# Performance work log

Measured on AMD Instinct MI355X. Metric: run time of the kernel, lower is better.

Reference implementation:

```python
import jax, jax.numpy as jnp
import numpy as np

K = 3      # deformable kernel size
PAD = 1    # padding for all 3x3 convs


def conv2d(x, w, b):
    y = jax.lax.conv_general_dilated(x, w, (1, 1), ((PAD, PAD), (PAD, PAD)),
                                     dimension_numbers=('NCHW', 'OIHW', 'NCHW'))
    return y + b[None, :, None, None]


def ln_channels(x, w, b, eps=1e-5):
    # Restormer 'WithBias' LayerNorm: normalize over channel dim of NCHW
    mu = jnp.mean(x, axis=1, keepdims=True)
    var = jnp.mean((x - mu) ** 2, axis=1, keepdims=True)
    return (x - mu) / jnp.sqrt(var + eps) * w[None, :, None, None] + b[None, :, None, None]


def deform_conv(x, offset, mask, weight, bias):
    # x: [B,Cin,H,W], offset: [B,2*K*K,H,W] (dy,dx interleaved), mask: [B,K*K,H,W]
    B, Cin, H, W = x.shape
    Kk = K * K
    off = offset.reshape(B, Kk, 2, H, W)
    dy, dx = off[:, :, 0], off[:, :, 1]                     # [B,Kk,H,W]
    ky, kx = jnp.meshgrid(jnp.arange(K), jnp.arange(K), indexing='ij')
    ky = (ky.reshape(-1) - PAD).astype(x.dtype)             # [Kk]
    kx = (kx.reshape(-1) - PAD).astype(x.dtype)
    py = jnp.arange(H, dtype=x.dtype)[None, None, :, None] + ky[None, :, None, None] + dy
    px = jnp.arange(W, dtype=x.dtype)[None, None, None, :] + kx[None, :, None, None] + dx
    y0 = jnp.floor(py); x0 = jnp.floor(px)
    wy1 = py - y0; wx1 = px - x0
    xf = x.reshape(B, Cin, H * W)

    def corner(yc, xc, wgt):
        valid = (yc >= 0) & (yc <= H - 1) & (xc >= 0) & (xc <= W - 1)
        yi = jnp.clip(yc, 0, H - 1).astype(jnp.int32)
        xi = jnp.clip(xc, 0, W - 1).astype(jnp.int32)
        idx = (yi * W + xi).reshape(B, -1)                  # [B, Kk*H*W]
        v = jax.vmap(lambda xb, ib: xb[:, ib])(xf, idx)     # [B, Cin, Kk*H*W]
        v = v.reshape(B, Cin, Kk, H, W)
        return v * (wgt * valid.astype(x.dtype))[:, None]

    sampled = (corner(y0, x0, (1 - wy1) * (1 - wx1))
               + corner(y0, x0 + 1, (1 - wy1) * wx1)
               + corner(y0 + 1, x0, wy1 * (1 - wx1))
               + corner(y0 + 1, x0 + 1, wy1 * wx1))         # [B,Cin,Kk,H,W]
    sampled = sampled * mask[:, None]                        # modulated (DCNv2)
    wk = weight.reshape(weight.shape[0], Cin, Kk)            # [Cout,Cin,Kk]
    out = jnp.einsum('bckhw,ock->bohw', sampled, wk)
    return out + bias[None, :, None, None]


def setup_inputs() -> dict:
    key = jax.random.key(0)
    ks = jax.random.split(key, 12)
    B, Ce, Cf, H, W = 4, 32, 64, 128, 128
    Cin, Kk = Ce + Cf, K * K
    d = {
        'f_evt_rec': jax.random.normal(ks[0], (B, Ce, H, W), jnp.float32),
        'f_efnet':   jax.random.normal(ks[1], (B, Cf, H, W), jnp.float32),
        'ln_evt_w': jnp.ones((Ce,), jnp.float32), 'ln_evt_b': jnp.zeros((Ce,), jnp.float32),
        'ln_ef_w':  jnp.ones((Cf,), jnp.float32), 'ln_ef_b':  jnp.zeros((Cf,), jnp.float32),
        'ln_al_w':  jnp.ones((Cf,), jnp.float32), 'ln_al_b':  jnp.zeros((Cf,), jnp.float32),
        'off_w': jax.random.normal(ks[2], (2 * Kk, Cin, K, K), jnp.float32) * 0.01,
        'off_b': jnp.zeros((2 * Kk,), jnp.float32),
        'mod_w': jax.random.normal(ks[3], (Kk, Cin, K, K), jnp.float32) * 0.01,
        'mod_b': jnp.zeros((Kk,), jnp.float32),
        'reg_w': jax.random.normal(ks[4], (Cf, Cin, K, K), jnp.float32) * 0.05,
        'reg_b': jnp.zeros((Cf,), jnp.float32),
        'stage_idx': 0,
    }
    return d


def reference(f_evt_rec, f_efnet, ln_evt_w, ln_evt_b, ln_ef_w, ln_ef_b,
              ln_al_w, ln_al_b, off_w, off_b, mod_w, mod_b, reg_w, reg_b, stage_idx):
    e = ln_channels(f_evt_rec, ln_evt_w, ln_evt_b)
    fe = ln_channels(f_efnet, ln_ef_w, ln_ef_b)
    ox = jnp.concatenate([e, fe], axis=1)                    # [B,96,H,W]
    offset = conv2d(ox, off_w, off_b)
    mask = 2.0 * jax.nn.sigmoid(conv2d(ox, mod_w, mod_b))
    al = deform_conv(ox, offset, mask, reg_w, reg_b)         # [B,64,H,W]
    al = jnp.where(al >= 0, al, 0.2 * al)                    # LeakyReLU(0.2)
    al = ln_channels(al, ln_al_w, ln_al_b)
    return al
```

## Files before the change

### kernel.cpp

```cpp
#include <hip/hip_runtime.h>
#include <hip/hip_bf16.h>

#define BATCH 4
#define HH 128
#define WW 128
#define CE 32
#define CF 64
#define CIN 96
#define KK 9
#define COUT 64

typedef __bf16 bf16x8 __attribute__((ext_vector_type(8)));
typedef float f32x4 __attribute__((ext_vector_type(4)));

#define MFMA16(a, b, c) __builtin_amdgcn_mfma_f32_16x16x32_bf16(a, b, c, 0, 0, 0)

typedef union { uint4 u; bf16x8 v; } U8;

#define OX_BYTES   (BATCH * HH * WW * CIN * 2)
#define OFFM_OFFB  OX_BYTES
#define OFFM_BYTES (BATCH * HH * WW * 27 * 4)
#define WCT_OFFB   (OFFM_OFFB + OFFM_BYTES)
#define WCT_BYTES  (32 * 864 * 2)
#define WKT_OFFB   (WCT_OFFB + WCT_BYTES)
#define WKT_BYTES  (64 * 864 * 2)

__global__ void prep_weights(const float* __restrict__ off_w,
                             const float* __restrict__ mod_w,
                             const float* __restrict__ reg_w,
                             __hip_bfloat16* __restrict__ wcombT,
                             __hip_bfloat16* __restrict__ wkT) {
  int e = blockIdx.x * 256 + threadIdx.x;
  const int TOT1 = 32 * 864;
  const int TOT2 = 64 * 864;
  if (e < TOT1) {
    int oc = e / 864, k = e % 864;
    int tap = k / 96, c = k % 96;
    float v = 0.f;
    if (oc < 18)      v = off_w[(oc * CIN + c) * KK + tap];
    else if (oc < 27) v = mod_w[((oc - 18) * CIN + c) * KK + tap];
    wcombT[e] = __float2bfloat16(v);
  } else if (e < TOT1 + TOT2) {
    int e2 = e - TOT1;
    int oc = e2 / 864, k = e2 % 864;
    int tap = k / 96, c = k % 96;
    wkT[e2] = __float2bfloat16(reg_w[(oc * CIN + c) * KK + tap]);
  }
}

__global__ __launch_bounds__(128) void ln_concat(
    const float* __restrict__ evt, const float* __restrict__ efn,
    const float* __restrict__ w_e, const float* __restrict__ b_e,
    const float* __restrict__ w_f, const float* __restrict__ b_f,
    __hip_bfloat16* __restrict__ ox) {
  __shared__ float vals[WW * 97];
  __shared__ float mu_e[WW], rs_e[WW], mu_f[WW], rs_f[WW];
  __shared__ float lnw[CIN], lnb[CIN];
  int t = threadIdx.x;
  int b = blockIdx.x >> 7, y = blockIdx.x & 127;
  if (t < CIN) {
    lnw[t] = (t < CE) ? w_e[t] : w_f[t - CE];
    lnb[t] = (t < CE) ? b_e[t] : b_f[t - CE];
  }
  int x = t;
  float s = 0.f, s2 = 0.f;
  const float* pe = evt + ((size_t)(b * CE) * HH + y) * WW + x;
  for (int c = 0; c < CE; ++c) {
    float v = pe[(size_t)c * HH * WW];
    vals[x * 97 + c] = v;
    s += v; s2 += v * v;
  }
  float mu = s * (1.f / CE);
  float var = s2 * (1.f / CE) - mu * mu;
  mu_e[x] = mu; rs_e[x] = rsqrtf(var + 1e-5f);
  s = 0.f; s2 = 0.f;
  const float* pf = efn + ((size_t)(b * CF) * HH + y) * WW + x;
  for (int c = 0; c < CF; ++c) {
    float v = pf[(size_t)c * HH * WW];
    vals[x * 97 + CE + c] = v;
    s += v; s2 += v * v;
  }
  mu = s * (1.f / CF);
  var = s2 * (1.f / CF) - mu * mu;
  mu_f[x] = mu; rs_f[x] = rsqrtf(var + 1e-5f);
  __syncthreads();
  uint* orow = (uint*)(ox + (size_t)blockIdx.x * WW * CIN);
  for (int i = 0; i < 48; ++i) {
    int g = i * 128 + t;
    int xx = g / 48, c = (g % 48) * 2;
    float v0 = vals[xx * 97 + c], v1 = vals[xx * 97 + c + 1];
    float o0 = (c < CE) ? (v0 - mu_e[xx]) * rs_e[xx] : (v0 - mu_f[xx]) * rs_f[xx];
    float o1 = (c + 1 < CE) ? (v1 - mu_e[xx]) * rs_e[xx] : (v1 - mu_f[xx]) * rs_f[xx];
    o0 = o0 * lnw[c] + lnb[c];
    o1 = o1 * lnw[c + 1] + lnb[c + 1];
    __hip_bfloat16 h0 = __float2bfloat16(o0), h1 = __float2bfloat16(o1);
    orow[g] = ((uint)*(unsigned short*)&h1 << 16) | (uint)*(unsigned short*)&h0;
  }
}

__global__ __launch_bounds__(256) void conv_offmask_mfma(
    const __hip_bfloat16* __restrict__ ox,
    const __hip_bfloat16* __restrict__ wcombT,
    const float* __restrict__ off_b, const float* __restrict__ mod_b,
    float* __restrict__ offm) {
  __shared__ float outl[64 * 28];

  int bid = blockIdx.x;
  int wg = (bid & 7) * 128 + (bid >> 3);
  int p0 = wg * 64;
  int b = p0 >> 14;
  int y = (p0 >> 7) & 127;
  int x0 = p0 & 127;

  int t = threadIdx.x, lane = t & 63, wv = t >> 6;
  int mw = wv >> 1, nw = wv & 1;
  int lr = lane & 15, lg = lane >> 4;

  const __hip_bfloat16* oxb = ox + (((size_t)b) << 14) * CIN;
  const __hip_bfloat16* brow = wcombT + (size_t)(nw * 16 + lr) * 864;

  f32x4 acc0 = {0.f, 0.f, 0.f, 0.f}, acc1 = {0.f, 0.f, 0.f, 0.f};

#pragma unroll
  for (int tap = 0; tap < 9; ++tap) {
    int dy = tap / 3 - 1, dx = tap % 3 - 1;
    int yy = y + dy;
    int xx0 = x0 + mw * 32 + lr + dx;
    int xx1 = xx0 + 16;
    bool v0 = ((unsigned)yy < 128u) && ((unsigned)xx0 < 128u);
    bool v1 = ((unsigned)yy < 128u) && ((unsigned)xx1 < 128u);
    int cy = min(max(yy, 0), 127);
    int cx0 = min(max(xx0, 0), 127);
    int cx1 = min(max(xx1, 0), 127);
    const __hip_bfloat16* arow = oxb + ((size_t)(cy << 7)) * CIN;
#pragma unroll
    for (int ks = 0; ks < 3; ++ks) {
      int ko = ks * 32 + lg * 8;
      U8 a0, a1, bf;
      a0.u = *(const uint4*)(arow + cx0 * CIN + ko);
      a1.u = *(const uint4*)(arow + cx1 * CIN + ko);
      if (!v0) { a0.u.x = 0; a0.u.y = 0; a0.u.z = 0; a0.u.w = 0; }
      if (!v1) { a1.u.x = 0; a1.u.y = 0; a1.u.z = 0; a1.u.w = 0; }
      bf.u = *(const uint4*)(brow + tap * 96 + ko);
      acc0 = MFMA16(a0.v, bf.v, acc0);
      acc1 = MFMA16(a1.v, bf.v, acc1);
    }
  }

  int oc = nw * 16 + lr;
  float bia = 0.f;
  if (oc < 18) bia = off_b[oc];
  else if (oc < 27) bia = mod_b[oc - 18];
#pragma unroll
  for (int mi = 0; mi < 2; ++mi) {
    f32x4 a = mi ? acc1 : acc0;
#pragma unroll
    for (int r = 0; r < 4; ++r) {
      int px = mw * 32 + mi * 16 + lg * 4 + r;
      if (oc < 27) {
        float v = a[r] + bia;
        if (oc >= 18) v = 2.f / (1.f + __expf(-v));
        outl[px * 28 + oc] = v;
      }
    }
  }
  __syncthreads();
  for (int e = t; e < 64 * 27; e += 256) {
    int px = e / 27, c = e % 27;
    offm[(size_t)p0 * 27 + e] = outl[px * 28 + c];
  }
}

__global__ __launch_bounds__(256) void deform_ln_mfma(
    const __hip_bfloat16* __restrict__ ox,
    const float* __restrict__ offm,
    const __hip_bfloat16* __restrict__ wkT,
    const float* __restrict__ reg_b,
    const float* __restrict__ lnw, const float* __restrict__ lnb,
    float* __restrict__ out) {
  __shared__ char smem[45056];
  int*   sI  = (int*)smem;
  float* sW  = (float*)(smem + 9216);
  short* SaA = (short*)(smem + 18432);
  short* SaB = (short*)(smem + 31744);
  float* outl = (float*)smem;

  int bid = blockIdx.x;
  int wg = (bid & 7) * 128 + (bid >> 3);
  int p0 = wg * 64;
  int b = p0 >> 14;
  int y = (p0 >> 7) & 127;
  int x0 = p0 & 127;
  const __hip_bfloat16* oxb = ox + (((size_t)b) << 14) * CIN;

  int t = threadIdx.x, lane = t & 63, wv = t >> 6;
  int mw = wv >> 1, nw = wv & 1;
  int lr = lane & 15, lg = lane >> 4;

  for (int u = t; u < 576; u += 256) {
    int px = u & 63, tap = u >> 6;
    const float* om = offm + (size_t)(p0 + px) * 27;
    float dyv = om[2 * tap], dxv = om[2 * tap + 1], mk = om[18 + tap];
    float psy = (float)(y + tap / 3 - 1) + dyv;
    float psx = (float)(x0 + px + tap % 3 - 1) + dxv;
    float fy = floorf(psy), fx = floorf(psx);
    float wy1 = psy - fy, wx1 = psx - fx;
    float wy0 = 1.f - wy1, wx0 = 1.f - wx1;
    int iy0 = (int)fy, ix0 = (int)fx;
    int iy1 = iy0 + 1, ix1 = ix0 + 1;
    float vy0 = ((unsigned)iy0 < 128u) ? 1.f : 0.f;
    float vy1 = ((unsigned)iy1 < 128u) ? 1.f : 0.f;
    float vx0 = ((unsigned)ix0 < 128u) ? 1.f : 0.f;
    float vx1 = ((unsigned)ix1 < 128u) ? 1.f : 0.f;
    int cy0 = min(max(iy0, 0), 127), cy1 = min(max(iy1, 0), 127);
    int cx0 = min(max(ix0, 0), 127), cx1 = min(max(ix1, 0), 127);
    int base = u * 4;
    sI[base + 0] = ((cy0 << 7) + cx0) * CIN;
    sI[base + 1] = ((cy0 << 7) + cx1) * CIN;
    sI[base + 2] = ((cy1 << 7) + cx0) * CIN;
    sI[base + 3] = ((cy1 << 7) + cx1) * CIN;
    sW[base + 0] = wy0 * wx0 * vy0 * vx0 * mk;
    sW[base + 1] = wy0 * wx1 * vy0 * vx1 * mk;
    sW[base + 2] = wy1 * wx0 * vy1 * vx0 * mk;
    sW[base + 3] = wy1 * wx1 * vy1 * vx1 * mk;
  }
  __syncthreads();

  f32x4 a00 = {0.f,0.f,0.f,0.f}, a01 = {0.f,0.f,0.f,0.f};
  f32x4 a10 = {0.f,0.f,0.f,0.f}, a11 = {0.f,0.f,0.f,0.f};

  const __hip_bfloat16* wb0 = wkT + (size_t)(nw * 32 + lr) * 864;
  const __hip_bfloat16* wb1 = wkT + (size_t)(nw * 32 + 16 + lr) * 864;

  for (int tap = 0; tap < 9; ++tap) {
    short* S = (tap & 1) ? SaB : SaA;
#pragma unroll
    for (int it = 0; it < 3; ++it) {
      int u = it * 256 + t;
      int px = u / 12, c8 = u % 12;
      int pb = (tap * 64 + px) * 4;
      const int* si = sI + pb;
      const float* sw = sW + pb;
      uint4 q0 = *(const uint4*)(oxb + si[0] + c8 * 8);
      uint4 q1 = *(const uint4*)(oxb + si[1] + c8 * 8);
      uint4 q2 = *(const uint4*)(oxb + si[2] + c8 * 8);
      uint4 q3 = *(const uint4*)(oxb + si[3] + c8 * 8);
      float w0 = sw[0], w1 = sw[1], w2 = sw[2], w3 = sw[3];
      uint rr[4];
#pragma unroll
      for (int j = 0; j < 4; ++j) {
        uint u0 = ((uint*)&q0)[j], u1 = ((uint*)&q1)[j];
        uint u2 = ((uint*)&q2)[j], u3 = ((uint*)&q3)[j];
        float lo = w0 * __uint_as_float(u0 << 16) + w1 * __uint_as_float(u1 << 16)
                 + w2 * __uint_as_float(u2 << 16) + w3 * __uint_as_float(u3 << 16);
        float hi = w0 * __uint_as_float(u0 & 0xffff0000u) + w1 * __uint_as_float(u1 & 0xffff0000u)
                 + w2 * __uint_as_float(u2 & 0xffff0000u) + w3 * __uint_as_float(u3 & 0xffff0000u);
        __hip_bfloat16 bl = __float2bfloat16(lo);
        __hip_bfloat16 bh = __float2bfloat16(hi);
        rr[j] = ((uint)*(unsigned short*)&bh << 16) | (uint)*(unsigned short*)&bl;
      }
      uint4 rv = {rr[0], rr[1], rr[2], rr[3]};
      *(uint4*)&S[px * 104 + c8 * 8] = rv;
    }
    __syncthreads();
#pragma unroll
    for (int ks = 0; ks < 3; ++ks) {
      int ko = ks * 32 + lg * 8;
      bf16x8 fa0 = *(const bf16x8*)&S[(mw * 32 + lr) * 104 + ko];
      bf16x8 fa1 = *(const bf16x8*)&S[(mw * 32 + 16 + lr) * 104 + ko];
      U8 b0, b1;
      b0.u = *(const uint4*)(wb0 + tap * 96 + ko);
      b1.u = *(const uint4*)(wb1 + tap * 96 + ko);
      a00 = MFMA16(fa0, b0.v, a00);
      a01 = MFMA16(fa0, b1.v, a01);
      a10 = MFMA16(fa1, b0.v, a10);
      a11 = MFMA16(fa1, b1.v, a11);
    }
  }
  __syncthreads();

#pragma unroll
  for (int mi = 0; mi < 2; ++mi)
#pragma unroll
  for (int ni = 0; ni < 2; ++ni) {
    int oc = nw * 32 + ni * 16 + lr;
    float bia = reg_b[oc];
    f32x4 a = (mi == 0) ? (ni == 0 ? a00 : a01) : (ni == 0 ? a10 : a11);
#pragma unroll
    for (int r = 0; r < 4; ++r) {
      int px = mw * 32 + mi * 16 + lg * 4 + r;
      float v = a[r] + bia;
      v = (v >= 0.f) ? v : 0.2f * v;
      outl[px * 68 + oc] = v;
    }
  }
  __syncthreads();

  {
    int px = t >> 2, part = t & 3;
    float s = 0.f, s2 = 0.f;
#pragma unroll
    for (int j = 0; j < 16; ++j) {
      float v = outl[px * 68 + part * 16 + j];
      s += v; s2 += v * v;
    }
    s += __shfl_xor(s, 1); s2 += __shfl_xor(s2, 1);
    s += __shfl_xor(s, 2); s2 += __shfl_xor(s2, 2);
    float mu = s * (1.f / 64.f);
    float var = s2 * (1.f / 64.f) - mu * mu;
    float rs = rsqrtf(var + 1e-5f);
    size_t ob = (size_t)b * COUT * 16384 + (size_t)y * 128 + x0 + px;
#pragma unroll
    for (int j = 0; j < 16; ++j) {
      int oc = part * 16 + j;
      float v = outl[px * 68 + oc];
      out[ob + (size_t)oc * 16384] = (v - mu) * rs * lnw[oc] + lnb[oc];
    }
  }
}

extern "C" void kernel_launch(void* const* d_in, const int* in_sizes, int n_in,
                              void* d_out, int out_size, void* d_ws, size_t ws_size,
                              hipStream_t stream) {
  const float* evt      = (const float*)d_in[0];
  const float* efn      = (const float*)d_in[1];
  const float* ln_evt_w = (const float*)d_in[2];
  const float* ln_evt_b = (const float*)d_in[3];
  const float* ln_ef_w  = (const float*)d_in[4];
  const float* ln_ef_b  = (const float*)d_in[5];
  const float* ln_al_w  = (const float*)d_in[6];
  const float* ln_al_b  = (const float*)d_in[7];
  const float* off_w    = (const float*)d_in[8];
  const float* off_b    = (const float*)d_in[9];
  const float* mod_w    = (const float*)d_in[10];
  const float* mod_b    = (const float*)d_in[11];
  const float* reg_w    = (const float*)d_in[12];
  const float* reg_b    = (const float*)d_in[13];
  float* out = (float*)d_out;

  char* wsb = (char*)d_ws;
  __hip_bfloat16* oxb    = (__hip_bfloat16*)wsb;
  float*          offm   = (float*)(wsb + OFFM_OFFB);
  __hip_bfloat16* wcombT = (__hip_bfloat16*)(wsb + WCT_OFFB);
  __hip_bfloat16* wkT    = (__hip_bfloat16*)(wsb + WKT_OFFB);

  prep_weights<<<(32 * 864 + 64 * 864 + 255) / 256, 256, 0, stream>>>(
      off_w, mod_w, reg_w, wcombT, wkT);
  ln_concat<<<BATCH * HH, 128, 0, stream>>>(
      evt, efn, ln_evt_w, ln_evt_b, ln_ef_w, ln_ef_b, oxb);
  conv_offmask_mfma<<<BATCH * HH * WW / 64, 256, 0, stream>>>(
      oxb, wcombT, off_b, mod_b, offm);
  deform_ln_mfma<<<BATCH * HH * WW / 64, 256, 0, stream>>>(
      oxb, offm, wkT, reg_b, ln_al_w, ln_al_b, out);
}
```

Before: 176.0 us.

## Fuse offset/mask conv into deformable conv kernel and software-pipeline bilinear gathers

Merges the offset/mask convolution and the deformable convolution into one kernel. The offset/mask results stay in shared memory instead of making a global round trip, and one launch is removed. The offset conv now reads a 3x66 halo tile of ox staged in LDS rather than issuing scattered global loads per tap. The deform gather is restructured so each thread handles one pixel and 24 channels, and the loads for the next tap are issued before the current tap's MFMAs. The LN/concat kernel is retiled to 64-pixel blocks with 256 threads and partial channel reductions. In exchange the fused kernel holds more registers and may run at lower occupancy.

```diff
diff --git a/kernel.cpp b/kernel.cpp
--- a/kernel.cpp
+++ b/kernel.cpp
@@ -12,18 +12,13 @@
 
 typedef __bf16 bf16x8 __attribute__((ext_vector_type(8)));
 typedef float f32x4 __attribute__((ext_vector_type(4)));
-
 #define MFMA16(a, b, c) __builtin_amdgcn_mfma_f32_16x16x32_bf16(a, b, c, 0, 0, 0)
-
 typedef union { uint4 u; bf16x8 v; } U8;
 
 #define OX_BYTES   (BATCH * HH * WW * CIN * 2)
-#define OFFM_OFFB  OX_BYTES
-#define OFFM_BYTES (BATCH * HH * WW * 27 * 4)
-#define WCT_OFFB   (OFFM_OFFB + OFFM_BYTES)
+#define WCT_OFFB   OX_BYTES
 #define WCT_BYTES  (32 * 864 * 2)
 #define WKT_OFFB   (WCT_OFFB + WCT_BYTES)
-#define WKT_BYTES  (64 * 864 * 2)
 
 __global__ void prep_weights(const float* __restrict__ off_w,
                              const float* __restrict__ mod_w,
@@ -48,220 +43,215 @@
   }
 }
 
-__global__ __launch_bounds__(128) void ln_concat(
+__global__ __launch_bounds__(256) void ln_concat(
     const float* __restrict__ evt, const float* __restrict__ efn,
     const float* __restrict__ w_e, const float* __restrict__ b_e,
     const float* __restrict__ w_f, const float* __restrict__ b_f,
     __hip_bfloat16* __restrict__ ox) {
-  __shared__ float vals[WW * 97];
-  __shared__ float mu_e[WW], rs_e[WW], mu_f[WW], rs_f[WW];
-  __shared__ float lnw[CIN], lnb[CIN];
-  int t = threadIdx.x;
-  int b = blockIdx.x >> 7, y = blockIdx.x & 127;
-  if (t < CIN) {
-    lnw[t] = (t < CE) ? w_e[t] : w_f[t - CE];
-    lnb[t] = (t < CE) ? b_e[t] : b_f[t - CE];
-  }
-  int x = t;
-  float s = 0.f, s2 = 0.f;
-  const float* pe = evt + ((size_t)(b * CE) * HH + y) * WW + x;
-  for (int c = 0; c < CE; ++c) {
-    float v = pe[(size_t)c * HH * WW];
-    vals[x * 97 + c] = v;
-    s += v; s2 += v * v;
-  }
-  float mu = s * (1.f / CE);
-  float var = s2 * (1.f / CE) - mu * mu;
-  mu_e[x] = mu; rs_e[x] = rsqrtf(var + 1e-5f);
-  s = 0.f; s2 = 0.f;
-  const float* pf = efn + ((size_t)(b * CF) * HH + y) * WW + x;
-  for (int c = 0; c < CF; ++c) {
-    float v = pf[(size_t)c * HH * WW];
-    vals[x * 97 + CE + c] = v;
-    s += v; s2 += v * v;
-  }
-  mu = s * (1.f / CF);
-  var = s2 * (1.f / CF) - mu * mu;
-  mu_f[x] = mu; rs_f[x] = rsqrtf(var + 1e-5f);
-  __syncthreads();
-  uint* orow = (uint*)(ox + (size_t)blockIdx.x * WW * CIN);
-  for (int i = 0; i < 48; ++i) {
-    int g = i * 128 + t;
-    int xx = g / 48, c = (g % 48) * 2;
-    float v0 = vals[xx * 97 + c], v1 = vals[xx * 97 + c + 1];
-    float o0 = (c < CE) ? (v0 - mu_e[xx]) * rs_e[xx] : (v0 - mu_f[xx]) * rs_f[xx];
-    float o1 = (c + 1 < CE) ? (v1 - mu_e[xx]) * rs_e[xx] : (v1 - mu_f[xx]) * rs_f[xx];
-    o0 = o0 * lnw[c] + lnb[c];
-    o1 = o1 * lnw[c + 1] + lnb[c + 1];
-    __hip_bfloat16 h0 = __float2bfloat16(o0), h1 = __float2bfloat16(o1);
-    orow[g] = ((uint)*(unsigned short*)&h1 << 16) | (uint)*(unsigned short*)&h0;
-  }
-}
-
-__global__ __launch_bounds__(256) void conv_offmask_mfma(
-    const __hip_bfloat16* __restrict__ ox,
-    const __hip_bfloat16* __restrict__ wcombT,
-    const float* __restrict__ off_b, const float* __restrict__ mod_b,
-    float* __restrict__ offm) {
-  __shared__ float outl[64 * 28];
+  __shared__ float vals[64 * 97];
+  __shared__ float part[4 * 64 * 4];
+  __shared__ float stat[64 * 4];
 
   int bid = blockIdx.x;
   int wg = (bid & 7) * 128 + (bid >> 3);
   int p0 = wg * 64;
-  int b = p0 >> 14;
-  int y = (p0 >> 7) & 127;
-  int x0 = p0 & 127;
+  int b = p0 >> 14, y = (p0 >> 7) & 127, x0 = p0 & 127;
+  int t = threadIdx.x, px = t & 63, g = t >> 6;
+
+  float sE = 0.f, sE2 = 0.f, sF = 0.f, sF2 = 0.f;
+  const float* pe = evt + (((size_t)b * CE) << 14) + (y << 7) + x0 + px;
+#pragma unroll
+  for (int j = 0; j < 8; ++j) {
+    int c = g * 8 + j;
+    float v = pe[(size_t)c << 14];
+    vals[px * 97 + c] = v; sE += v; sE2 += v * v;
+  }
+  const float* pf = efn + (((size_t)b * CF) << 14) + (y << 7) + x0 + px;
+#pragma unroll
+  for (int j = 0; j < 16; ++j) {
+    int c = g * 16 + j;
+    float v = pf[(size_t)c << 14];
+    vals[px * 97 + CE + c] = v; sF += v; sF2 += v * v;
+  }
+  {
+    float4 p4 = {sE, sE2, sF, sF2};
+    *(float4*)&part[(g * 64 + px) * 4] = p4;
+  }
+  __syncthreads();
+  if (g == 0) {
+    float aE = 0.f, aE2 = 0.f, aF = 0.f, aF2 = 0.f;
+#pragma unroll
+    for (int gg = 0; gg < 4; ++gg) {
+      float4 p4 = *(const float4*)&part[(gg * 64 + px) * 4];
+      aE += p4.x; aE2 += p4.y; aF += p4.z; aF2 += p4.w;
+    }
+    float muE = aE * (1.f / CE);
+    float vE = aE2 * (1.f / CE) - muE * muE;
+    float muF = aF * (1.f / CF);
+    float vF = aF2 * (1.f / CF) - muF * muF;
+    float4 s4 = {muE, rsqrtf(vE + 1e-5f), muF, rsqrtf(vF + 1e-5f)};
+    *(float4*)&stat[px * 4] = s4;
+  }
+  __syncthreads();
+  uint* orow = (uint*)(ox + (size_t)p0 * CIN);
+#pragma unroll
+  for (int i = 0; i < 12; ++i) {
+    int e = i * 256 + t;
+    int xx = e / 48, c = (e % 48) * 2;
+    float v0 = vals[xx * 97 + c], v1 = vals[xx * 97 + c + 1];
+    float mu, rs, lw0, lb0, lw1, lb1;
+    if (c < CE) {
+      mu = stat[xx * 4 + 0]; rs = stat[xx * 4 + 1];
+      lw0 = w_e[c]; lb0 = b_e[c]; lw1 = w_e[c + 1]; lb1 = b_e[c + 1];
+    } else {
+      mu = stat[xx * 4 + 2]; rs = stat[xx * 4 + 3];
+      lw0 = w_f[c - CE]; lb0 = b_f[c - CE]; lw1 = w_f[c + 1 - CE]; lb1 = b_f[c + 1 - CE];
+    }
+    float o0 = (v0 - mu) * rs * lw0 + lb0;
+    float o1 = (v1 - mu) * rs * lw1 + lb1;
+    __hip_bfloat16 h0 = __float2bfloat16(o0), h1 = __float2bfloat16(o1);
+    orow[e] = ((uint)*(unsigned short*)&h1 << 16) | (uint)*(unsigned short*)&h0;
+  }
+}
+
+__device__ __forceinline__ uint blend1(uint u0, uint u1, uint u2, uint u3,
+                                       float w0, float w1, float w2, float w3) {
+  float lo = w0 * __uint_as_float(u0 << 16) + w1 * __uint_as_float(u1 << 16)
+           + w2 * __uint_as_float(u2 << 16) + w3 * __uint_as_float(u3 << 16);
+  float hi = w0 * __uint_as_float(u0 & 0xffff0000u) + w1 * __uint_as_float(u1 & 0xffff0000u)
+           + w2 * __uint_as_float(u2 & 0xffff0000u) + w3 * __uint_as_float(u3 & 0xffff0000u);
+  __hip_bfloat16 bl = __float2bfloat16(lo), bh = __float2bfloat16(hi);
+  return ((uint)*(unsigned short*)&bh << 16) | (uint)*(unsigned short*)&bl;
+}
+
+__global__ __launch_bounds__(256) void conv_deform_fused(
+    const __hip_bfloat16* __restrict__ ox,
+    const __hip_bfloat16* __restrict__ wcombT,
+    const __hip_bfloat16* __restrict__ wkT,
+    const float* __restrict__ off_b, const float* __restrict__ mod_b,
+    const float* __restrict__ reg_b,
+    const float* __restrict__ lnw, const float* __restrict__ lnb,
+    float* __restrict__ out) {
+  __shared__ char smem[41216];
+  short* At   = (short*)smem;
+  float* offm = (float*)smem;
+  short* SaA  = (short*)(smem + 7168);
+  short* SaB  = (short*)(smem + 20480);
+  float* outl = (float*)(smem + 7168);
+
+  int bid = blockIdx.x;
+  int wg = (bid & 7) * 128 + (bid >> 3);
+  int p0 = wg * 64;
+  int b = p0 >> 14, y = (p0 >> 7) & 127, x0 = p0 & 127;
+  const __hip_bfloat16* oxb = ox + (((size_t)b) << 14) * CIN;
 
   int t = threadIdx.x, lane = t & 63, wv = t >> 6;
   int mw = wv >> 1, nw = wv & 1;
   int lr = lane & 15, lg = lane >> 4;
 
-  const __hip_bfloat16* oxb = ox + (((size_t)b) << 14) * CIN;
-  const __hip_bfloat16* brow = wcombT + (size_t)(nw * 16 + lr) * 864;
-
-  f32x4 acc0 = {0.f, 0.f, 0.f, 0.f}, acc1 = {0.f, 0.f, 0.f, 0.f};
-
-#pragma unroll
-  for (int tap = 0; tap < 9; ++tap) {
-    int dy = tap / 3 - 1, dx = tap % 3 - 1;
-    int yy = y + dy;
-    int xx0 = x0 + mw * 32 + lr + dx;
-    int xx1 = xx0 + 16;
-    bool v0 = ((unsigned)yy < 128u) && ((unsigned)xx0 < 128u);
-    bool v1 = ((unsigned)yy < 128u) && ((unsigned)xx1 < 128u);
-    int cy = min(max(yy, 0), 127);
-    int cx0 = min(max(xx0, 0), 127);
-    int cx1 = min(max(xx1, 0), 127);
-    const __hip_bfloat16* arow = oxb + ((size_t)(cy << 7)) * CIN;
-#pragma unroll
-    for (int ks = 0; ks < 3; ++ks) {
-      int ko = ks * 32 + lg * 8;
-      U8 a0, a1, bf;
-      a0.u = *(const uint4*)(arow + cx0 * CIN + ko);
-      a1.u = *(const uint4*)(arow + cx1 * CIN + ko);
-      if (!v0) { a0.u.x = 0; a0.u.y = 0; a0.u.z = 0; a0.u.w = 0; }
-      if (!v1) { a1.u.x = 0; a1.u.y = 0; a1.u.z = 0; a1.u.w = 0; }
-      bf.u = *(const uint4*)(brow + tap * 96 + ko);
-      acc0 = MFMA16(a0.v, bf.v, acc0);
-      acc1 = MFMA16(a1.v, bf.v, acc1);
-    }
-  }
-
-  int oc = nw * 16 + lr;
-  float bia = 0.f;
-  if (oc < 18) bia = off_b[oc];
-  else if (oc < 27) bia = mod_b[oc - 18];
-#pragma unroll
-  for (int mi = 0; mi < 2; ++mi) {
-    f32x4 a = mi ? acc1 : acc0;
-#pragma unroll
-    for (int r = 0; r < 4; ++r) {
-      int px = mw * 32 + mi * 16 + lg * 4 + r;
-      if (oc < 27) {
-        float v = a[r] + bia;
-        if (oc >= 18) v = 2.f / (1.f + __expf(-v));
-        outl[px * 28 + oc] = v;
+  for (int u = t; u < 3 * 66 * 12; u += 256) {
+    int c8 = u % 12, pw_ = u / 12, w = pw_ % 66, r = pw_ / 66;
+    int yy = y + r - 1, xx = x0 + w - 1;
+    uint4 v = {0u, 0u, 0u, 0u};
+    if ((unsigned)yy < 128u && (unsigned)xx < 128u)
+      v = *(const uint4*)(oxb + (size_t)((yy << 7) + xx) * CIN + c8 * 8);
+    *(uint4*)&At[(r * 66 + w) * 104 + c8 * 8] = v;
+  }
+  __syncthreads();
+
+  f32x4 cc0 = {0.f,0.f,0.f,0.f}, cc1 = {0.f,0.f,0.f,0.f};
+  {
+    const __hip_bfloat16* brow = wcombT + (size_t)(nw * 16 + lr) * 864;
+#pragma unroll
+    for (int tap = 0; tap < 9; ++tap) {
+      int dy = tap / 3, dx = tap % 3;
+#pragma unroll
+      for (int ks = 0; ks < 3; ++ks) {
+        int ko = ks * 32 + lg * 8;
+        bf16x8 a0 = *(const bf16x8*)&At[(dy * 66 + mw * 32 + lr + dx) * 104 + ko];
+        bf16x8 a1 = *(const bf16x8*)&At[(dy * 66 + mw * 32 + 16 + lr + dx) * 104 + ko];
+        U8 bf; bf.u = *(const uint4*)(brow + tap * 96 + ko);
+        cc0 = MFMA16(a0, bf.v, cc0);
+        cc1 = MFMA16(a1, bf.v, cc1);
       }
     }
   }
   __syncthreads();
-  for (int e = t; e < 64 * 27; e += 256) {
-    int px = e / 27, c = e % 27;
-    offm[(size_t)p0 * 27 + e] = outl[px * 28 + c];
-  }
-}
-
-__global__ __launch_bounds__(256) void deform_ln_mfma(
-    const __hip_bfloat16* __restrict__ ox,
-    const float* __restrict__ offm,
-    const __hip_bfloat16* __restrict__ wkT,
-    const float* __restrict__ reg_b,
-    const float* __restrict__ lnw, const float* __restrict__ lnb,
-    float* __restrict__ out) {
-  __shared__ char smem[45056];
-  int*   sI  = (int*)smem;
-  float* sW  = (float*)(smem + 9216);
-  short* SaA = (short*)(smem + 18432);
-  short* SaB = (short*)(smem + 31744);
-  float* outl = (float*)smem;
-
-  int bid = blockIdx.x;
-  int wg = (bid & 7) * 128 + (bid >> 3);
-  int p0 = wg * 64;
-  int b = p0 >> 14;
-  int y = (p0 >> 7) & 127;
-  int x0 = p0 & 127;
-  const __hip_bfloat16* oxb = ox + (((size_t)b) << 14) * CIN;
-
-  int t = threadIdx.x, lane = t & 63, wv = t >> 6;
-  int mw = wv >> 1, nw = wv & 1;
-  int lr = lane & 15, lg = lane >> 4;
-
-  for (int u = t; u < 576; u += 256) {
-    int px = u & 63, tap = u >> 6;
-    const float* om = offm + (size_t)(p0 + px) * 27;
-    float dyv = om[2 * tap], dxv = om[2 * tap + 1], mk = om[18 + tap];
-    float psy = (float)(y + tap / 3 - 1) + dyv;
-    float psx = (float)(x0 + px + tap % 3 - 1) + dxv;
-    float fy = floorf(psy), fx = floorf(psx);
-    float wy1 = psy - fy, wx1 = psx - fx;
-    float wy0 = 1.f - wy1, wx0 = 1.f - wx1;
-    int iy0 = (int)fy, ix0 = (int)fx;
-    int iy1 = iy0 + 1, ix1 = ix0 + 1;
-    float vy0 = ((unsigned)iy0 < 128u) ? 1.f : 0.f;
-    float vy1 = ((unsigned)iy1 < 128u) ? 1.f : 0.f;
-    float vx0 = ((unsigned)ix0 < 128u) ? 1.f : 0.f;
-    float vx1 = ((unsigned)ix1 < 128u) ? 1.f : 0.f;
-    int cy0 = min(max(iy0, 0), 127), cy1 = min(max(iy1, 0), 127);
-    int cx0 = min(max(ix0, 0), 127), cx1 = min(max(ix1, 0), 127);
-    int base = u * 4;
-    sI[base + 0] = ((cy0 << 7) + cx0) * CIN;
-    sI[base + 1] = ((cy0 << 7) + cx1) * CIN;
-    sI[base + 2] = ((cy1 << 7) + cx0) * CIN;
-    sI[base + 3] = ((cy1 << 7) + cx1) * CIN;
-    sW[base + 0] = wy0 * wx0 * vy0 * vx0 * mk;
-    sW[base + 1] = wy0 * wx1 * vy0 * vx1 * mk;
-    sW[base + 2] = wy1 * wx0 * vy1 * vx0 * mk;
-    sW[base + 3] = wy1 * wx1 * vy1 * vx1 * mk;
-  }
-  __syncthreads();
-
+
+  {
+    int oc = nw * 16 + lr;
+    if (oc < 27) {
+      float bia = (oc < 18) ? off_b[oc] : mod_b[oc - 18];
+#pragma unroll
+      for (int mi = 0; mi < 2; ++mi) {
+        f32x4 a = mi ? cc1 : cc0;
+#pragma unroll
+        for (int r = 0; r < 4; ++r) {
+          int px2 = mw * 32 + mi * 16 + lg * 4 + r;
+          float v = a[r] + bia;
+          if (oc >= 18) v = 2.f / (1.f + __expf(-v));
+          offm[px2 * 28 + oc] = v;
+        }
+      }
+    }
+  }
+  __syncthreads();
+
+  int px = t & 63;
+  int c8b = wv * 3;
+  const __hip_bfloat16* gb = oxb + c8b * 8;
+  const __hip_bfloat16* wb0 = wkT + (size_t)(nw * 32 + lr) * 864;
+  const __hip_bfloat16* wb1 = wkT + (size_t)(nw * 32 + 16 + lr) * 864;
   f32x4 a00 = {0.f,0.f,0.f,0.f}, a01 = {0.f,0.f,0.f,0.f};
   f32x4 a10 = {0.f,0.f,0.f,0.f}, a11 = {0.f,0.f,0.f,0.f};
 
-  const __hip_bfloat16* wb0 = wkT + (size_t)(nw * 32 + lr) * 864;
-  const __hip_bfloat16* wb1 = wkT + (size_t)(nw * 32 + 16 + lr) * 864;
-
+  uint4 qa0,qa1,qa2,qa3, qb0,qb1,qb2,qb3, qc0,qc1,qc2,qc3;
+  float pw0, pw1, pw2, pw3;
+
+#define ISSUE(TAP)                                                           \
+  {                                                                          \
+    const float* om = offm + px * 28;                                        \
+    float dyv = om[2 * (TAP)], dxv = om[2 * (TAP) + 1], mk = om[18 + (TAP)]; \
+    float psy = (float)(y + (TAP) / 3 - 1) + dyv;                            \
+    float psx = (float)(x0 + px + (TAP) % 3 - 1) + dxv;                      \
+    float fy = floorf(psy), fx = floorf(psx);                                \
+    float wy1 = psy - fy, wx1 = psx - fx;                                    \
+    float wy0 = 1.f - wy1, wx0 = 1.f - wx1;                                  \
+    int iy0 = (int)fy, ix0 = (int)fx, iy1 = iy0 + 1, ix1 = ix0 + 1;          \
+    float vy0 = ((unsigned)iy0 < 128u) ? 1.f : 0.f;                          \
+    float vy1 = ((unsigned)iy1 < 128u) ? 1.f : 0.f;                          \
+    float vx0 = ((unsigned)ix0 < 128u) ? 1.f : 0.f;                          \
+    float vx1 = ((unsigned)ix1 < 128u) ? 1.f : 0.f;                          \
+    int cy0 = min(max(iy0, 0), 127), cy1 = min(max(iy1, 0), 127);            \
+    int cx0 = min(max(ix0, 0), 127), cx1 = min(max(ix1, 0), 127);            \
+    int i00 = ((cy0 << 7) + cx0) * CIN, i01 = ((cy0 << 7) + cx1) * CIN;      \
+    int i10 = ((cy1 << 7) + cx0) * CIN, i11 = ((cy1 << 7) + cx1) * CIN;      \
+    pw0 = wy0 * wx0 * vy0 * vx0 * mk; pw1 = wy0 * wx1 * vy0 * vx1 * mk;      \
+    pw2 = wy1 * wx0 * vy1 * vx0 * mk; pw3 = wy1 * wx1 * vy1 * vx1 * mk;      \
+    qa0 = *(const uint4*)(gb + i00);      qa1 = *(const uint4*)(gb + i01);   \
+    qa2 = *(const uint4*)(gb + i10);      qa3 = *(const uint4*)(gb + i11);   \
+    qb0 = *(const uint4*)(gb + i00 + 8);  qb1 = *(const uint4*)(gb + i01 + 8); \
+    qb2 = *(const uint4*)(gb + i10 + 8);  qb3 = *(const uint4*)(gb + i11 + 8); \
+    qc0 = *(const uint4*)(gb + i00 + 16); qc1 = *(const uint4*)(gb + i01 + 16);\
+    qc2 = *(const uint4*)(gb + i10 + 16); qc3 = *(const uint4*)(gb + i11 + 16);\
+  }
+
+#define BLEND(Q0, Q1, Q2, Q3, DST)                                           \
+  { uint4 rv;                                                                \
+    rv.x = blend1(Q0.x, Q1.x, Q2.x, Q3.x, pw0, pw1, pw2, pw3);               \
+    rv.y = blend1(Q0.y, Q1.y, Q2.y, Q3.y, pw0, pw1, pw2, pw3);               \
+    rv.z = blend1(Q0.z, Q1.z, Q2.z, Q3.z, pw0, pw1, pw2, pw3);               \
+    rv.w = blend1(Q0.w, Q1.w, Q2.w, Q3.w, pw0, pw1, pw2, pw3);               \
+    *(uint4*)&(DST) = rv; }
+
+  ISSUE(0);
+  int buf = 0;
   for (int tap = 0; tap < 9; ++tap) {
-    short* S = (tap & 1) ? SaB : SaA;
-#pragma unroll
-    for (int it = 0; it < 3; ++it) {
-      int u = it * 256 + t;
-      int px = u / 12, c8 = u % 12;
-      int pb = (tap * 64 + px) * 4;
-      const int* si = sI + pb;
-      const float* sw = sW + pb;
-      uint4 q0 = *(const uint4*)(oxb + si[0] + c8 * 8);
-      uint4 q1 = *(const uint4*)(oxb + si[1] + c8 * 8);
-      uint4 q2 = *(const uint4*)(oxb + si[2] + c8 * 8);
-      uint4 q3 = *(const uint4*)(oxb + si[3] + c8 * 8);
-      float w0 = sw[0], w1 = sw[1], w2 = sw[2], w3 = sw[3];
-      uint rr[4];
-#pragma unroll
-      for (int j = 0; j < 4; ++j) {
-        uint u0 = ((uint*)&q0)[j], u1 = ((uint*)&q1)[j];
-        uint u2 = ((uint*)&q2)[j], u3 = ((uint*)&q3)[j];
-        float lo = w0 * __uint_as_float(u0 << 16) + w1 * __uint_as_float(u1 << 16)
-                 + w2 * __uint_as_float(u2 << 16) + w3 * __uint_as_float(u3 << 16);
-        float hi = w0 * __uint_as_float(u0 & 0xffff0000u) + w1 * __uint_as_float(u1 & 0xffff0000u)
-                 + w2 * __uint_as_float(u2 & 0xffff0000u) + w3 * __uint_as_float(u3 & 0xffff0000u);
-        __hip_bfloat16 bl = __float2bfloat16(lo);
-        __hip_bfloat16 bh = __float2bfloat16(hi);
-        rr[j] = ((uint)*(unsigned short*)&bh << 16) | (uint)*(unsigned short*)&bl;
-      }
-      uint4 rv = {rr[0], rr[1], rr[2], rr[3]};
-      *(uint4*)&S[px * 104 + c8 * 8] = rv;
-    }
+    short* S = buf ? SaB : SaA;
+    BLEND(qa0, qa1, qa2, qa3, S[px * 104 + (c8b + 0) * 8]);
+    BLEND(qb0, qb1, qb2, qb3, S[px * 104 + (c8b + 1) * 8]);
+    BLEND(qc0, qc1, qc2, qc3, S[px * 104 + (c8b + 2) * 8]);
+    if (tap < 8) ISSUE(tap + 1);
     __syncthreads();
 #pragma unroll
     for (int ks = 0; ks < 3; ++ks) {
@@ -276,6 +266,7 @@
       a10 = MFMA16(fa1, b0.v, a10);
       a11 = MFMA16(fa1, b1.v, a11);
     }
+    buf ^= 1;
   }
   __syncthreads();
 
@@ -288,20 +279,19 @@
     f32x4 a = (mi == 0) ? (ni == 0 ? a00 : a01) : (ni == 0 ? a10 : a11);
 #pragma unroll
     for (int r = 0; r < 4; ++r) {
-      int px = mw * 32 + mi * 16 + lg * 4 + r;
+      int px2 = mw * 32 + mi * 16 + lg * 4 + r;
       float v = a[r] + bia;
       v = (v >= 0.f) ? v : 0.2f * v;
-      outl[px * 68 + oc] = v;
-    }
-  }
-  __syncthreads();
-
+      outl[px2 * 68 + oc] = v;
+    }
+  }
+  __syncthreads();
   {
-    int px = t >> 2, part = t & 3;
+    int px2 = t >> 2, part = t & 3;
     float s = 0.f, s2 = 0.f;
 #pragma unroll
     for (int j = 0; j < 16; ++j) {
-      float v = outl[px * 68 + part * 16 + j];
+      float v = outl[px2 * 68 + part * 16 + j];
       s += v; s2 += v * v;
     }
     s += __shfl_xor(s, 1); s2 += __shfl_xor(s2, 1);
@@ -309,14 +299,16 @@
     float mu = s * (1.f / 64.f);
     float var = s2 * (1.f / 64.f) - mu * mu;
     float rs = rsqrtf(var + 1e-5f);
-    size_t ob = (size_t)b * COUT * 16384 + (size_t)y * 128 + x0 + px;
+    size_t ob = (size_t)b * COUT * 16384 + (size_t)y * 128 + x0 + px2;
 #pragma unroll
     for (int j = 0; j < 16; ++j) {
       int oc = part * 16 + j;
-      float v = outl[px * 68 + oc];
+      float v = outl[px2 * 68 + oc];
       out[ob + (size_t)oc * 16384] = (v - mu) * rs * lnw[oc] + lnb[oc];
     }
   }
+#undef ISSUE
+#undef BLEND
 }
 
 extern "C" void kernel_launch(void* const* d_in, const int* in_sizes, int n_in,
@@ -340,16 +332,13 @@
 
   char* wsb = (char*)d_ws;
   __hip_bfloat16* oxb    = (__hip_bfloat16*)wsb;
-  float*          offm   = (float*)(wsb + OFFM_OFFB);
   __hip_bfloat16* wcombT = (__hip_bfloat16*)(wsb + WCT_OFFB);
   __hip_bfloat16* wkT    = (__hip_bfloat16*)(wsb + WKT_OFFB);
 
   prep_weights<<<(32 * 864 + 64 * 864 + 255) / 256, 256, 0, stream>>>(
       off_w, mod_w, reg_w, wcombT, wkT);
-  ln_concat<<<BATCH * HH, 128, 0, stream>>>(
+  ln_concat<<<BATCH * HH * WW / 64, 256, 0, stream>>>(
       evt, efn, ln_evt_w, ln_evt_b, ln_ef_w, ln_ef_b, oxb);
-  conv_offmask_mfma<<<BATCH * HH * WW / 64, 256, 0, stream>>>(
-      oxb, wcombT, off_b, mod_b, offm);
-  deform_ln_mfma<<<BATCH * HH * WW / 64, 256, 0, stream>>>(
-      oxb, offm, wkT, reg_b, ln_al_w, ln_al_b, out);
-}
+  conv_deform_fused<<<BATCH * HH * WW / 64, 256, 0, stream>>>(
+      oxb, wcombT, wkT, off_b, mod_b, reg_b, ln_al_w, ln_al_b, out);
+}
```

Measured after the change: 174.6 us. No clear change (-0.8%).
